# Kernel optimization log

Measured on AMD Instinct MI355X. Metric: run time of the kernel, lower is better.

The kernel has to match this reference:

```python
import jax, jax.numpy as jnp
import numpy as np

NUM_ENT = 100000
DIM = 768
BATCH = 4096
TAU = 0.05
ALPHA = 0.5
LARGE_NUM = 1e9


def setup_inputs() -> dict:
    key = jax.random.key(0)
    k1, k2 = jax.random.split(key)
    emb = jax.random.normal(k1, (NUM_ENT, DIM), dtype=jnp.float32)
    train_links = jax.random.randint(k2, (BATCH, 2), 0, NUM_ENT, dtype=jnp.int64)
    return {"emb": emb, "train_links": train_links}


def _soft_xent(logits, batch_size):
    # target is one-hot on column i for row i -> pick diagonal of log_softmax
    logprobs = jax.nn.log_softmax(logits, axis=1)
    diag = logprobs[jnp.arange(batch_size), jnp.arange(batch_size)]
    return -jnp.sum(diag) / batch_size


def reference(emb, train_links):
    # L2-normalize embeddings (norm=True default)
    emb_n = emb / jnp.linalg.norm(emb, axis=1, keepdims=True)
    h1 = emb_n[train_links[:, 0]]  # [B, D]
    h2 = emb_n[train_links[:, 1]]  # [B, D]
    B = h1.shape[0]
    mask = jnp.eye(B, dtype=h1.dtype) * LARGE_NUM

    logits_aa = jnp.matmul(h1, h1.T) / TAU - mask  # [B, B]
    logits_bb = jnp.matmul(h2, h2.T) / TAU - mask
    logits_ab = jnp.matmul(h1, h2.T) / TAU
    logits_ba = jnp.matmul(h2, h1.T) / TAU

    logits_a = jnp.concatenate([logits_ab, logits_aa], axis=1)  # [B, 2B]
    logits_b = jnp.concatenate([logits_ba, logits_bb], axis=1)

    loss_a = _soft_xent(logits_a, B)
    loss_b = _soft_xent(logits_b, B)
    return ALPHA * loss_a + (1.0 - ALPHA) * loss_b
```

## Files before the change

kernel.cpp:

```cpp
#include <hip/hip_runtime.h>
#include <hip/hip_bf16.h>
#include <math.h>

#define NUM_ENT 100000
#define DIM 768
#define BATCH 4096
#define INV_TAU 20.0f

typedef __attribute__((ext_vector_type(8))) short short8;
typedef __attribute__((ext_vector_type(4))) float f32x4;

__global__ __launch_bounds__(256) void gather_norm(
    const float* __restrict__ emb, const int* __restrict__ links,
    __hip_bfloat16* __restrict__ hn1, __hip_bfloat16* __restrict__ hn2)
{
    int rowId = blockIdx.x;
    int b     = rowId >> 1;
    int which = rowId & 1;
    int src   = links[2 * b + which];
    const float* srcRow = emb + (size_t)src * DIM;

    int t = threadIdx.x;
    float4 v = make_float4(0.f, 0.f, 0.f, 0.f);
    float ss = 0.f;
    if (t < DIM / 4) {
        v = ((const float4*)srcRow)[t];
        ss = v.x * v.x + v.y * v.y + v.z * v.z + v.w * v.w;
    }
    #pragma unroll
    for (int off = 32; off >= 1; off >>= 1) ss += __shfl_xor(ss, off);
    __shared__ float wsum[4];
    if ((t & 63) == 0) wsum[t >> 6] = ss;
    __syncthreads();
    float tot = wsum[0] + wsum[1] + wsum[2] + wsum[3];
    float scale = 1.0f / sqrtf(tot);

    if (t < DIM / 4) {
        __hip_bfloat16* dst = (which ? hn2 : hn1) + (size_t)b * DIM;
        union { ushort4 u; __hip_bfloat16 h[4]; } o;
        o.h[0] = __float2bfloat16(v.x * scale);
        o.h[1] = __float2bfloat16(v.y * scale);
        o.h[2] = __float2bfloat16(v.z * scale);
        o.h[3] = __float2bfloat16(v.w * scale);
        ((ushort4*)dst)[t] = o.u;
    }
}

__global__ __launch_bounds__(256) void gram_sym(
    const __hip_bfloat16* __restrict__ hn1, const __hip_bfloat16* __restrict__ hn2,
    float* __restrict__ S, float* __restrict__ diag)
{
    const int ct = blockIdx.x;
    const int rt = blockIdx.y;
    const int matId = blockIdx.z;
    if (matId > 0 && ct < rt) return;

    const __hip_bfloat16* A  = (matId == 2) ? hn2 : hn1;
    const __hip_bfloat16* Bm = (matId == 1) ? hn1 : hn2;
    const int  rowTarget = (matId == 2) ? 1 : 0;
    const int  colTarget = (matId == 1) ? 0 : 1;
    const bool maskDiag  = (matId > 0) && (rt == ct);
    const bool doColsum  = (matId == 0) || (rt != ct);
    const bool captureDiag = (matId == 0);

    __shared__ short sA[128 * 32];
    __shared__ short sB[128 * 32];

    const int t    = threadIdx.x;
    const int lane = t & 63;
    const int wave = t >> 6;
    const int wm   = wave >> 1, wn = wave & 1;
    const int quad = lane >> 4, l16 = lane & 15;
    const int row0 = rt * 128;
    const int col0 = ct * 128;

    f32x4 acc[4][4];
    #pragma unroll
    for (int im = 0; im < 4; ++im)
        #pragma unroll
        for (int jn = 0; jn < 4; ++jn)
            acc[im][jn] = (f32x4){0.f, 0.f, 0.f, 0.f};

    for (int kk = 0; kk < DIM; kk += 32) {
        #pragma unroll
        for (int i = 0; i < 2; ++i) {
            int c  = i * 256 + t;
            int r  = c >> 2;
            int s  = c & 3;
            int q8 = (((s - (r >> 1)) & 3)) * 8;
            const __hip_bfloat16* ga = A  + (size_t)(row0 + r) * DIM + kk + q8;
            const __hip_bfloat16* gb = Bm + (size_t)(col0 + r) * DIM + kk + q8;
            __builtin_amdgcn_global_load_lds(
                (const __attribute__((address_space(1))) void*)ga,
                (__attribute__((address_space(3))) void*)(sA + c * 8), 16, 0, 0);
            __builtin_amdgcn_global_load_lds(
                (const __attribute__((address_space(1))) void*)gb,
                (__attribute__((address_space(3))) void*)(sB + c * 8), 16, 0, 0);
        }
        __syncthreads();

        short8 af[4], bfr[4];
        #pragma unroll
        for (int im = 0; im < 4; ++im) {
            int row = wm * 64 + im * 16 + l16;
            int slot = (quad + (row >> 1)) & 3;
            af[im] = *(const short8*)&sA[row * 32 + slot * 8];
        }
        #pragma unroll
        for (int jn = 0; jn < 4; ++jn) {
            int row = wn * 64 + jn * 16 + l16;
            int slot = (quad + (row >> 1)) & 3;
            bfr[jn] = *(const short8*)&sB[row * 32 + slot * 8];
        }

        #pragma unroll
        for (int im = 0; im < 4; ++im)
            #pragma unroll
            for (int jn = 0; jn < 4; ++jn)
                acc[im][jn] = __builtin_amdgcn_mfma_f32_16x16x32_bf16(
                    af[im], bfr[jn], acc[im][jn], 0, 0, 0);
        __syncthreads();
    }

    float csum[4] = {0.f, 0.f, 0.f, 0.f};
    #pragma unroll
    for (int im = 0; im < 4; ++im) {
        #pragma unroll
        for (int r = 0; r < 4; ++r) {
            const int gi = row0 + wm * 64 + im * 16 + quad * 4 + r;
            float rsum = 0.f;
            #pragma unroll
            for (int jn = 0; jn < 4; ++jn) {
                const int gj = col0 + wn * 64 + jn * 16 + l16;
                float logit = acc[im][jn][r] * INV_TAU;
                bool isDiag = (gi == gj);
                if (captureDiag && isDiag) diag[gi] = logit;
                float e = __expf(logit);
                if (maskDiag && isDiag) e = 0.f;
                rsum += e;
                csum[jn] += e;
            }
            rsum += __shfl_xor(rsum, 1);
            rsum += __shfl_xor(rsum, 2);
            rsum += __shfl_xor(rsum, 4);
            rsum += __shfl_xor(rsum, 8);
            if (l16 == 0) atomicAdd(&S[rowTarget * BATCH + gi], rsum);
        }
    }
    if (doColsum) {
        #pragma unroll
        for (int jn = 0; jn < 4; ++jn) {
            float c = csum[jn];
            c += __shfl_xor(c, 16);
            c += __shfl_xor(c, 32);
            if (quad == 0) {
                const int gj = col0 + wn * 64 + jn * 16 + l16;
                atomicAdd(&S[colTarget * BATCH + gj], c);
            }
        }
    }
}

__global__ __launch_bounds__(256) void finalize(
    const float* __restrict__ S, const float* __restrict__ diag,
    float* __restrict__ out)
{
    int t = threadIdx.x;
    float local = 0.f;
    for (int i = t; i < BATCH; i += 256) {
        float lse_a = logf(S[i]);
        float lse_b = logf(S[BATCH + i]);
        local += 0.5f * (lse_a + lse_b) - diag[i];
    }
    #pragma unroll
    for (int off = 32; off >= 1; off >>= 1) local += __shfl_xor(local, off);
    __shared__ float wsum[4];
    if ((t & 63) == 0) wsum[t >> 6] = local;
    __syncthreads();
    if (t == 0) out[0] = (wsum[0] + wsum[1] + wsum[2] + wsum[3]) / (float)BATCH;
}

extern "C" void kernel_launch(void* const* d_in, const int* in_sizes, int n_in,
                              void* d_out, int out_size, void* d_ws, size_t ws_size,
                              hipStream_t stream)
{
    const float* emb  = (const float*)d_in[0];
    const int* links  = (const int*)d_in[1];

    char* ws = (char*)d_ws;
    __hip_bfloat16* hn1 = (__hip_bfloat16*)ws;
    __hip_bfloat16* hn2 = (__hip_bfloat16*)(ws + (size_t)BATCH * DIM * 2);
    float* S    = (float*)(ws + (size_t)BATCH * DIM * 4);
    float* diag = (float*)(ws + (size_t)BATCH * DIM * 4 + 2 * BATCH * 4);

    hipMemsetAsync(S, 0, 2 * BATCH * sizeof(float), stream);

    gather_norm<<<dim3(2 * BATCH), 256, 0, stream>>>(emb, links, hn1, hn2);
    gram_sym<<<dim3(32, 32, 3), 256, 0, stream>>>(hn1, hn2, S, diag);
    finalize<<<1, 256, 0, stream>>>(S, diag, (float*)d_out);
}
```

Before: 445.6 us.

## Fuse three Gram products into one symmetric 8192x8192 Gram with double buffering

Concatenates h1 and h2 into one 8192-row matrix Z and computes only the upper triangle of Z·Zᵀ with 128x256 tiles. Each entry feeds both row and column sums, and the tiles that straddle the diagonal mask the lower part. The K loop is double-buffered in LDS so the next slice's global loads overlap the MFMAs, with one barrier per step. The gather kernel now uses one wave per row and no shared-memory reduction. The larger tiles raise register and LDS pressure, and tiles on the diagonal waste part of their work.

```diff
diff --git a/kernel.cpp b/kernel.cpp
--- a/kernel.cpp
+++ b/kernel.cpp
@@ -10,133 +10,129 @@
 typedef __attribute__((ext_vector_type(8))) short short8;
 typedef __attribute__((ext_vector_type(4))) float f32x4;
 
-__global__ __launch_bounds__(256) void gather_norm(
+__global__ __launch_bounds__(64) void gather_norm(
     const float* __restrict__ emb, const int* __restrict__ links,
-    __hip_bfloat16* __restrict__ hn1, __hip_bfloat16* __restrict__ hn2)
+    __hip_bfloat16* __restrict__ Z)
 {
     int rowId = blockIdx.x;
     int b     = rowId >> 1;
     int which = rowId & 1;
     int src   = links[2 * b + which];
-    const float* srcRow = emb + (size_t)src * DIM;
+    const float4* srcRow = (const float4*)(emb + (size_t)src * DIM);
 
     int t = threadIdx.x;
-    float4 v = make_float4(0.f, 0.f, 0.f, 0.f);
+    float4 v[3];
     float ss = 0.f;
-    if (t < DIM / 4) {
-        v = ((const float4*)srcRow)[t];
-        ss = v.x * v.x + v.y * v.y + v.z * v.z + v.w * v.w;
+    #pragma unroll
+    for (int j = 0; j < 3; ++j) {
+        v[j] = srcRow[t + 64 * j];
+        ss += v[j].x*v[j].x + v[j].y*v[j].y + v[j].z*v[j].z + v[j].w*v[j].w;
     }
     #pragma unroll
     for (int off = 32; off >= 1; off >>= 1) ss += __shfl_xor(ss, off);
-    __shared__ float wsum[4];
-    if ((t & 63) == 0) wsum[t >> 6] = ss;
-    __syncthreads();
-    float tot = wsum[0] + wsum[1] + wsum[2] + wsum[3];
-    float scale = 1.0f / sqrtf(tot);
+    float scale = rsqrtf(ss);
 
-    if (t < DIM / 4) {
-        __hip_bfloat16* dst = (which ? hn2 : hn1) + (size_t)b * DIM;
+    __hip_bfloat16* dst = Z + (size_t)(which * BATCH + b) * DIM;
+    #pragma unroll
+    for (int j = 0; j < 3; ++j) {
         union { ushort4 u; __hip_bfloat16 h[4]; } o;
-        o.h[0] = __float2bfloat16(v.x * scale);
-        o.h[1] = __float2bfloat16(v.y * scale);
-        o.h[2] = __float2bfloat16(v.z * scale);
-        o.h[3] = __float2bfloat16(v.w * scale);
-        ((ushort4*)dst)[t] = o.u;
+        o.h[0] = __float2bfloat16(v[j].x * scale);
+        o.h[1] = __float2bfloat16(v[j].y * scale);
+        o.h[2] = __float2bfloat16(v[j].z * scale);
+        o.h[3] = __float2bfloat16(v[j].w * scale);
+        ((ushort4*)dst)[t + 64 * j] = o.u;
     }
 }
 
-__global__ __launch_bounds__(256) void gram_sym(
-    const __hip_bfloat16* __restrict__ hn1, const __hip_bfloat16* __restrict__ hn2,
+__global__ __launch_bounds__(256, 2) void gram_fused(
+    const __hip_bfloat16* __restrict__ Z,
     float* __restrict__ S, float* __restrict__ diag)
 {
-    const int ct = blockIdx.x;
-    const int rt = blockIdx.y;
-    const int matId = blockIdx.z;
-    if (matId > 0 && ct < rt) return;
+    const int tj = blockIdx.x;
+    const int ti = blockIdx.y;
+    if (ti > 2 * tj + 1) return;
+    const bool straddle = ((ti >> 1) == tj);
 
-    const __hip_bfloat16* A  = (matId == 2) ? hn2 : hn1;
-    const __hip_bfloat16* Bm = (matId == 1) ? hn1 : hn2;
-    const int  rowTarget = (matId == 2) ? 1 : 0;
-    const int  colTarget = (matId == 1) ? 0 : 1;
-    const bool maskDiag  = (matId > 0) && (rt == ct);
-    const bool doColsum  = (matId == 0) || (rt != ct);
-    const bool captureDiag = (matId == 0);
-
-    __shared__ short sA[128 * 32];
-    __shared__ short sB[128 * 32];
+    __shared__ short sA[2][128 * 32];
+    __shared__ short sB[2][256 * 32];
 
     const int t    = threadIdx.x;
     const int lane = t & 63;
     const int wave = t >> 6;
-    const int wm   = wave >> 1, wn = wave & 1;
+    const int wr   = wave >> 1, wc = wave & 1;
     const int quad = lane >> 4, l16 = lane & 15;
-    const int row0 = rt * 128;
-    const int col0 = ct * 128;
+    const int row0 = ti * 128;
+    const int col0 = tj * 256;
 
-    f32x4 acc[4][4];
+    f32x4 acc[4][8];
     #pragma unroll
     for (int im = 0; im < 4; ++im)
         #pragma unroll
-        for (int jn = 0; jn < 4; ++jn)
+        for (int jn = 0; jn < 8; ++jn)
             acc[im][jn] = (f32x4){0.f, 0.f, 0.f, 0.f};
 
-    for (int kk = 0; kk < DIM; kk += 32) {
+    auto issue = [&](int bi, int kk) {
         #pragma unroll
         for (int i = 0; i < 2; ++i) {
-            int c  = i * 256 + t;
-            int r  = c >> 2;
-            int s  = c & 3;
-            int q8 = (((s - (r >> 1)) & 3)) * 8;
-            const __hip_bfloat16* ga = A  + (size_t)(row0 + r) * DIM + kk + q8;
-            const __hip_bfloat16* gb = Bm + (size_t)(col0 + r) * DIM + kk + q8;
+            int c = i * 256 + t, r = c >> 2, s = c & 3;
+            int q8 = ((s - (r >> 1)) & 3) * 8;
+            const __hip_bfloat16* g = Z + (size_t)(row0 + r) * DIM + kk + q8;
             __builtin_amdgcn_global_load_lds(
-                (const __attribute__((address_space(1))) void*)ga,
-                (__attribute__((address_space(3))) void*)(sA + c * 8), 16, 0, 0);
+                (const __attribute__((address_space(1))) void*)g,
+                (__attribute__((address_space(3))) void*)(&sA[bi][c * 8]), 16, 0, 0);
+        }
+        #pragma unroll
+        for (int i = 0; i < 4; ++i) {
+            int c = i * 256 + t, r = c >> 2, s = c & 3;
+            int q8 = ((s - (r >> 1)) & 3) * 8;
+            const __hip_bfloat16* g = Z + (size_t)(col0 + r) * DIM + kk + q8;
             __builtin_amdgcn_global_load_lds(
-                (const __attribute__((address_space(1))) void*)gb,
-                (__attribute__((address_space(3))) void*)(sB + c * 8), 16, 0, 0);
+                (const __attribute__((address_space(1))) void*)g,
+                (__attribute__((address_space(3))) void*)(&sB[bi][c * 8]), 16, 0, 0);
         }
+    };
+
+    issue(0, 0);
+    for (int it = 0; it < DIM / 32; ++it) {
+        const int cur = it & 1;
         __syncthreads();
+        if (it + 1 < DIM / 32) issue(cur ^ 1, (it + 1) * 32);
 
-        short8 af[4], bfr[4];
+        short8 af[4], bf[8];
         #pragma unroll
         for (int im = 0; im < 4; ++im) {
-            int row = wm * 64 + im * 16 + l16;
+            int row  = wr * 64 + im * 16 + l16;
             int slot = (quad + (row >> 1)) & 3;
-            af[im] = *(const short8*)&sA[row * 32 + slot * 8];
+            af[im] = *(const short8*)&sA[cur][row * 32 + slot * 8];
         }
         #pragma unroll
-        for (int jn = 0; jn < 4; ++jn) {
-            int row = wn * 64 + jn * 16 + l16;
+        for (int jn = 0; jn < 8; ++jn) {
+            int row  = wc * 128 + jn * 16 + l16;
             int slot = (quad + (row >> 1)) & 3;
-            bfr[jn] = *(const short8*)&sB[row * 32 + slot * 8];
+            bf[jn] = *(const short8*)&sB[cur][row * 32 + slot * 8];
         }
-
         #pragma unroll
         for (int im = 0; im < 4; ++im)
             #pragma unroll
-            for (int jn = 0; jn < 4; ++jn)
+            for (int jn = 0; jn < 8; ++jn)
                 acc[im][jn] = __builtin_amdgcn_mfma_f32_16x16x32_bf16(
-                    af[im], bfr[jn], acc[im][jn], 0, 0, 0);
-        __syncthreads();
+                    af[im], bf[jn], acc[im][jn], 0, 0, 0);
     }
 
-    float csum[4] = {0.f, 0.f, 0.f, 0.f};
+    float csum[8] = {0.f, 0.f, 0.f, 0.f, 0.f, 0.f, 0.f, 0.f};
     #pragma unroll
     for (int im = 0; im < 4; ++im) {
         #pragma unroll
         for (int r = 0; r < 4; ++r) {
-            const int gi = row0 + wm * 64 + im * 16 + quad * 4 + r;
+            const int gi = row0 + wr * 64 + im * 16 + quad * 4 + r;
             float rsum = 0.f;
             #pragma unroll
-            for (int jn = 0; jn < 4; ++jn) {
-                const int gj = col0 + wn * 64 + jn * 16 + l16;
+            for (int jn = 0; jn < 8; ++jn) {
+                const int gj = col0 + wc * 128 + jn * 16 + l16;
                 float logit = acc[im][jn][r] * INV_TAU;
-                bool isDiag = (gi == gj);
-                if (captureDiag && isDiag) diag[gi] = logit;
+                if (gj - BATCH == gi) diag[gi] = logit;
                 float e = __expf(logit);
-                if (maskDiag && isDiag) e = 0.f;
+                if (straddle && gi >= gj) e = 0.f;
                 rsum += e;
                 csum[jn] += e;
             }
@@ -144,19 +140,17 @@
             rsum += __shfl_xor(rsum, 2);
             rsum += __shfl_xor(rsum, 4);
             rsum += __shfl_xor(rsum, 8);
-            if (l16 == 0) atomicAdd(&S[rowTarget * BATCH + gi], rsum);
+            if (l16 == 0) atomicAdd(&S[gi], rsum);
         }
     }
-    if (doColsum) {
-        #pragma unroll
-        for (int jn = 0; jn < 4; ++jn) {
-            float c = csum[jn];
-            c += __shfl_xor(c, 16);
-            c += __shfl_xor(c, 32);
-            if (quad == 0) {
-                const int gj = col0 + wn * 64 + jn * 16 + l16;
-                atomicAdd(&S[colTarget * BATCH + gj], c);
-            }
+    #pragma unroll
+    for (int jn = 0; jn < 8; ++jn) {
+        float c = csum[jn];
+        c += __shfl_xor(c, 16);
+        c += __shfl_xor(c, 32);
+        if (quad == 0) {
+            const int gj = col0 + wc * 128 + jn * 16 + l16;
+            atomicAdd(&S[gj], c);
         }
     }
 }
@@ -188,14 +182,13 @@
     const int* links  = (const int*)d_in[1];
 
     char* ws = (char*)d_ws;
-    __hip_bfloat16* hn1 = (__hip_bfloat16*)ws;
-    __hip_bfloat16* hn2 = (__hip_bfloat16*)(ws + (size_t)BATCH * DIM * 2);
-    float* S    = (float*)(ws + (size_t)BATCH * DIM * 4);
-    float* diag = (float*)(ws + (size_t)BATCH * DIM * 4 + 2 * BATCH * 4);
+    __hip_bfloat16* Z = (__hip_bfloat16*)ws;
+    float* S    = (float*)(ws + (size_t)2 * BATCH * DIM * 2);
+    float* diag = (float*)(ws + (size_t)2 * BATCH * DIM * 2 + 2 * BATCH * 4);
 
     hipMemsetAsync(S, 0, 2 * BATCH * sizeof(float), stream);
 
-    gather_norm<<<dim3(2 * BATCH), 256, 0, stream>>>(emb, links, hn1, hn2);
-    gram_sym<<<dim3(32, 32, 3), 256, 0, stream>>>(hn1, hn2, S, diag);
+    gather_norm<<<dim3(2 * BATCH), 64, 0, stream>>>(emb, links, Z);
+    gram_fused<<<dim3(32, 64), 256, 0, stream>>>(Z, S, diag);
     finalize<<<1, 256, 0, stream>>>(S, diag, (float*)d_out);
 }
```

Result: slower. 474.6 us (+6.5%).
